# Kernel optimization log

Measured on AMD Instinct MI355X. Metric: run time of the kernel, lower is better.

Reference implementation:

```python
import jax, jax.numpy as jnp
import numpy as np

B, NCH, NPTS, NGT = 8, 4, 1024, 10
NANCH = 5 * NPTS
NMIN, NMAX = 64, 64
M = NMIN + NMAX
NPOOL = 64
EXT = 0.2
EPS = 1e-5
PERM = np.array([3, 4, 5, 1, 0, 2, 6])

_C = jnp.array([[0., 1, 0], [0, -1, 0], [2.5, -1, 0], [2.5, 1, 0], [2.5, 0, 0]], jnp.float32)
_ROT = jnp.array([[1., 0, 0], [0, 0, 1], [0, 1, 0]], jnp.float32)  # theta=0 rotation from source
NEW_CENTERS = _C @ _ROT  # (5,3)
DIM = jnp.array([2., 2., 5.], jnp.float32)


def _conv1x1(x, w, b):
    return jnp.einsum('bci,oc->boi', x, w) + b[None, :, None]


def _bn(x, g, be):  # BatchNorm1d in train mode: batch stats over (N, L)
    m = x.mean((0, 2), keepdims=True)
    v = ((x - m) ** 2).mean((0, 2), keepdims=True)
    return (x - m) * jax.lax.rsqrt(v + EPS) * g[None, :, None] + be[None, :, None]


def _corners(b):  # b=(cx,cz,w,l,ry) -> (4,2) CCW BEV corners
    lx = jnp.array([0.5, -0.5, -0.5, 0.5]) * b[2]
    lz = jnp.array([0.5, 0.5, -0.5, -0.5]) * b[3]
    c, s = jnp.cos(b[4]), jnp.sin(b[4])
    return jnp.stack([b[0] + lx * c - lz * s, b[1] + lx * s + lz * c], 1)


def _clip(poly, count, e1, e2):  # Sutherland-Hodgman: clip convex poly (8,2) by left half-plane of e1->e2
    idx = jnp.arange(8)
    valid = idx < count
    cnt = jnp.maximum(count, 1)
    nxt = poly[(idx + 1) % cnt]
    ex, ez = e2[0] - e1[0], e2[1] - e1[1]
    dc = ex * (poly[:, 1] - e1[1]) - ez * (poly[:, 0] - e1[0])
    dn = ex * (nxt[:, 1] - e1[1]) - ez * (nxt[:, 0] - e1[0])
    in_c, in_n = dc >= 0, dn >= 0
    den = dc - dn
    t = dc / jnp.where(jnp.abs(den) < 1e-9, 1e-9, den)
    inter = poly + t[:, None] * (nxt - poly)
    flags = jnp.stack([valid & in_c, valid & (in_c ^ in_n)], 1).reshape(16)
    pts = jnp.stack([poly, inter], 1).reshape(16, 2)
    pos = jnp.cumsum(flags) - 1
    out = jnp.zeros((8, 2), poly.dtype).at[jnp.where(flags, pos, 8)].set(pts, mode='drop')
    return out, flags.sum()


def _bev_iou(a, b):  # rotated BEV IoU, a,b=(cx,cz,w,l,ry)
    poly = jnp.zeros((8, 2)).at[:4].set(_corners(a))
    count = jnp.int32(4)
    cb = _corners(b)
    for k in range(4):
        poly, count = _clip(poly, count, cb[k], cb[(k + 1) % 4])
    idx = jnp.arange(8)
    nxt = poly[(idx + 1) % jnp.maximum(count, 1)]
    inter = 0.5 * jnp.abs(jnp.sum(jnp.where(idx < count, poly[:, 0] * nxt[:, 1] - nxt[:, 0] * poly[:, 1], 0.)))
    return inter / jnp.maximum(a[2] * a[3] + b[2] * b[3] - inter, 1e-8)


def _bev(b7):  # (..,7)=[x,y,z,h,w,l,ry] -> (cx,cz,w,l,ry)
    return jnp.stack([b7[..., 0], b7[..., 2], b7[..., 4], b7[..., 5], b7[..., 6]], -1)


def _select_one(pnts, labels):  # pnts (N,3), labels (G,9)
    cent = (pnts[:, None, :] - NEW_CENTERS[None]).reshape(NANCH, 3)  # repeat_interleave(pnts,5)-tile(centers)
    anchors = jnp.concatenate([jnp.broadcast_to(DIM, (NANCH, 3)), cent, jnp.zeros((NANCH, 1))], 1)
    a7 = anchors[:, PERM]
    g7 = labels[:, PERM]
    ab, gb = _bev(a7), _bev(g7)
    iou2d = jax.vmap(lambda g: jax.vmap(lambda a: _bev_iou(g, a))(ab))(gb)  # (G, NANCH)
    max_iou = iou2d.max(0)
    max_ind = jnp.argmax(iou2d, 0)
    order = jnp.argsort(max_iou)
    sel = jnp.concatenate([order[:NMIN], order[-NMAX:]])  # bottom-k + top-k
    return a7[sel], max_ind[sel], max_iou[sel]


def _pool_one(box, pts, ft):  # roipool3d: first NPOOL points inside expanded box, zero-padded
    c, s = jnp.cos(box[6]), jnp.sin(box[6])
    dx, dz = pts[:, 0] - box[0], pts[:, 2] - box[2]
    xl = dx * c + dz * s
    zl = -dx * s + dz * c
    inside = (jnp.abs(xl) < box[4] * 0.5 + EXT) & (jnp.abs(zl) < box[5] * 0.5 + EXT) \
             & (pts[:, 1] > box[1] - box[3] - EXT) & (pts[:, 1] < box[1] + EXT)
    order = jnp.argsort(jnp.logical_not(inside))[:NPOOL]  # stable sort: inside points first, original order
    valid = inside[order].astype(ft.dtype)[:, None]
    return jnp.concatenate([ft[order], pts[order]], -1) * valid  # (NPOOL, 256+3)


def _forward(points, gt_labels, p):
    x = jax.nn.relu(_bn(_conv1x1(points, p['pn_w1'], p['pn_b1']), p['pn_g1'], p['pn_be1']))
    x = jax.nn.relu(_bn(_conv1x1(x, p['pn_w2'], p['pn_b2']), p['pn_g2'], p['pn_be2']))
    x = _bn(_conv1x1(x, p['pn_w3'], p['pn_b3']), p['pn_g3'], p['pn_be3'])  # (B,256,N)
    pts = jnp.transpose(points[:, :3, :], (0, 2, 1))  # (B,N,3)
    sel_boxes, sel_idx, sel_iou = jax.vmap(_select_one)(pts, gt_labels)  # (B,M,7),(B,M),(B,M)
    ftr = jnp.transpose(x, (0, 2, 1))  # (B,N,256)
    pooled = jax.vmap(lambda bx, pp, ff: jax.vmap(lambda b: _pool_one(b, pp, ff))(bx))(sel_boxes, pts, ftr)
    pooled = pooled - jnp.pad(sel_boxes[:, :, None, :3], ((0, 0), (0, 0), (0, 0), (256, 0)))  # subtract center from last 3 ch
    pf = jnp.transpose(pooled.reshape(B * M, NPOOL, 259), (0, 2, 1))  # (B*M,259,64)
    f = _bn(_conv1x1(pf, p['rp_w1'], p['rp_b1']), p['rp_g1'], p['rp_be1'])
    f = _bn(_conv1x1(f, p['rp_w2'], p['rp_b2']), p['rp_g2'], p['rp_be2'])
    feats = f.reshape(B, M, 1024, NPOOL).max(-1)
    labels_bin = (sel_iou > 0.5).astype(jnp.int32)
    return feats, labels_bin, sel_iou, sel_boxes, gt_labels[-1], sel_idx


def setup_inputs():
    key = jax.random.key(0)
    ks = jax.random.split(key, 16)
    points = jax.random.normal(ks[0], (B, NCH, NPTS), jnp.float32) * 3.0
    dims = jax.random.uniform(ks[1], (B, NGT, 3), minval=1.0, maxval=4.0)
    ctrs = jax.random.normal(ks[2], (B, NGT, 3)) * 3.0
    th = jax.random.uniform(ks[3], (B, NGT, 1), minval=-3.14, maxval=3.14)
    extra = jax.random.normal(ks[4], (B, NGT, 2))
    gt_labels = jnp.concatenate([dims, ctrs, th, extra], -1).astype(jnp.float32)  # (B,G,9)
    inp = {'points': points, 'gt_labels': gt_labels}
    shapes = [('pn', 1, 64, NCH), ('pn', 2, 128, 64), ('pn', 3, 256, 128), ('rp', 1, 512, 259), ('rp', 2, 1024, 512)]
    for j, (pre, n, o, i) in enumerate(shapes):
        inp[f'{pre}_w{n}'] = jax.random.normal(ks[5 + j], (o, i), jnp.float32) / np.sqrt(i).astype(np.float32)
        inp[f'{pre}_b{n}'] = jnp.zeros((o,), jnp.float32)
        inp[f'{pre}_g{n}'] = jnp.ones((o,), jnp.float32)
        inp[f'{pre}_be{n}'] = jnp.zeros((o,), jnp.float32)
    return inp


def reference(points, gt_labels, pn_w1, pn_b1, pn_g1, pn_be1, pn_w2, pn_b2, pn_g2, pn_be2, pn_w3, pn_b3, pn_g3, pn_be3, rp_w1, rp_b1, rp_g1, rp_be1, rp_w2, rp_b2, rp_g2, rp_be2):
    p = dict(pn_w1=pn_w1, pn_b1=pn_b1, pn_g1=pn_g1, pn_be1=pn_be1, pn_w2=pn_w2, pn_b2=pn_b2, pn_g2=pn_g2, pn_be2=pn_be2, pn_w3=pn_w3, pn_b3=pn_b3, pn_g3=pn_g3, pn_be3=pn_be3, rp_w1=rp_w1, rp_b1=rp_b1, rp_g1=rp_g1, rp_be1=rp_be1, rp_w2=rp_w2, rp_b2=rp_b2, rp_g2=rp_g2, rp_be2=rp_be2)
    return _forward(points, gt_labels, p)
```

## Files before the change

kernel.cpp:

```cpp
#include <hip/hip_runtime.h>
#include <hip/hip_bf16.h>
#include <float.h>
#include <math.h>


typedef __attribute__((ext_vector_type(8))) short short8;
typedef __attribute__((ext_vector_type(4))) float f32x4;

template <int CTRL>
__device__ __forceinline__ float dppmv(float x) {
  return __int_as_float(__builtin_amdgcn_update_dpp(
      0, __float_as_int(x), CTRL, 0xF, 0xF, true));
}
__device__ __forceinline__ float dpp_sum16(float x) {
  x += dppmv<0xB1>(x);
  x += dppmv<0x4E>(x);
  x += dppmv<0x124>(x);
  x += dppmv<0x128>(x);
  return x;
}

__device__ __forceinline__ void stage1k(const unsigned short* g, unsigned short* l) {
  __builtin_amdgcn_global_load_lds(
      (const __attribute__((address_space(1))) unsigned int*)g,
      (__attribute__((address_space(3))) unsigned int*)l, 16, 0, 0);
}

#define FMA16()                                                                 \
  do {                                                                          \
    float4 av = *(const float4*)&sWT[cc][to * 4];                               \
    float4 bv = *(const float4*)&sB[cc][tk * 4];                                \
    acc[0][0] = fmaf(av.x, bv.x, acc[0][0]);                                    \
    acc[0][1] = fmaf(av.x, bv.y, acc[0][1]);                                    \
    acc[0][2] = fmaf(av.x, bv.z, acc[0][2]);                                    \
    acc[0][3] = fmaf(av.x, bv.w, acc[0][3]);                                    \
    acc[1][0] = fmaf(av.y, bv.x, acc[1][0]);                                    \
    acc[1][1] = fmaf(av.y, bv.y, acc[1][1]);                                    \
    acc[1][2] = fmaf(av.y, bv.z, acc[1][2]);                                    \
    acc[1][3] = fmaf(av.y, bv.w, acc[1][3]);                                    \
    acc[2][0] = fmaf(av.z, bv.x, acc[2][0]);                                    \
    acc[2][1] = fmaf(av.z, bv.y, acc[2][1]);                                    \
    acc[2][2] = fmaf(av.z, bv.z, acc[2][2]);                                    \
    acc[2][3] = fmaf(av.z, bv.w, acc[2][3]);                                    \
    acc[3][0] = fmaf(av.w, bv.x, acc[3][0]);                                    \
    acc[3][1] = fmaf(av.w, bv.y, acc[3][1]);                                    \
    acc[3][2] = fmaf(av.w, bv.z, acc[3][2]);                                    \
    acc[3][3] = fmaf(av.w, bv.w, acc[3][3]);                                    \
  } while (0)

template <int C, int O, bool AFF, bool RELU, bool TRANS>
__global__ __launch_bounds__(256) void conv_pn(const float* __restrict__ in,
                                               const float* __restrict__ w,
                                               const float* __restrict__ bias,
                                               const float* __restrict__ aff,
                                               float* __restrict__ out) {
  __shared__ __align__(16) float sB[64][68];
  __shared__ __align__(16) float sWT[64][68];
  const int i0 = blockIdx.x * 64;
  const int o0 = blockIdx.y * 64;
  const int b = blockIdx.z;
  const int tid = threadIdx.x;
  const int tk = tid & 15, to = tid >> 4;
  float acc[4][4] = {};
  for (int c0 = 0; c0 < C; c0 += 64) {
    const int cs = (C - c0 < 64) ? (C - c0) : 64;
    for (int idx = tid; idx < 4096; idx += 256) {
      int ii = idx & 63, cc = idx >> 6;
      float v = 0.f;
      if (cc < cs) {
        int c = c0 + cc;
        v = in[(b * C + c) * 1024 + i0 + ii];
        if (AFF) v = fmaf(v, aff[c], aff[C + c]);
        if (RELU) v = fmaxf(v, 0.f);
      }
      sB[cc][ii] = v;
    }
    for (int idx = tid; idx < 4096; idx += 256) {
      int cc = idx & 63, oo = idx >> 6;
      sWT[cc][oo] = (cc < cs) ? w[(o0 + oo) * C + c0 + cc] : 0.f;
    }
    __syncthreads();
    for (int cc = 0; cc < cs; ++cc) { FMA16(); }
    __syncthreads();
  }
  if (TRANS) {
    float b0 = bias[o0 + to * 4], b1 = bias[o0 + to * 4 + 1];
    float b2 = bias[o0 + to * 4 + 2], b3 = bias[o0 + to * 4 + 3];
#pragma unroll
    for (int jj = 0; jj < 4; ++jj) {
      float4 v = make_float4(acc[0][jj] + b0, acc[1][jj] + b1, acc[2][jj] + b2, acc[3][jj] + b3);
      *(float4*)&out[((size_t)(b * 1024) + i0 + tk * 4 + jj) * O + o0 + to * 4] = v;
    }
  } else {
    for (int j = 0; j < 4; ++j) {
      int o = o0 + to * 4 + j;
      float bs = bias[o];
      float4 v = make_float4(acc[j][0] + bs, acc[j][1] + bs, acc[j][2] + bs, acc[j][3] + bs);
      *(float4*)&out[(b * O + o) * 1024 + i0 + tk * 4] = v;
    }
  }
}

__global__ __launch_bounds__(256) void bn_stats(const float* __restrict__ x,
                                                const float* __restrict__ g,
                                                const float* __restrict__ be,
                                                float* __restrict__ aff, int C) {
#pragma clang fp contract(off)
  int c = blockIdx.x;
  int tid = threadIdx.x;
  float s = 0.f, q = 0.f;
  for (int idx = tid; idx < 8192; idx += 256) {
    int b = idx >> 10, i = idx & 1023;
    float v = x[(b * C + c) * 1024 + i];
    s += v;
    q += v * v;
  }
  for (int m = 1; m < 64; m <<= 1) {
    s += __shfl_xor(s, m);
    q += __shfl_xor(q, m);
  }
  __shared__ float as_[4], aq_[4];
  int wv = tid >> 6;
  if ((tid & 63) == 0) { as_[wv] = s; aq_[wv] = q; }
  __syncthreads();
  if (tid == 0) {
    s = as_[0] + as_[1] + as_[2] + as_[3];
    q = aq_[0] + aq_[1] + aq_[2] + aq_[3];
    float m_ = s * (1.f / 8192.f);
    float var = q * (1.f / 8192.f) - m_ * m_;
    float A = g[c] / sqrtf(var + 1e-5f);
    aff[c] = A;
    aff[C + c] = be[c] - m_ * A;
  }
}

__global__ __launch_bounds__(256) void bn_stats_t(const float* __restrict__ x,
                                                  const float* __restrict__ g,
                                                  const float* __restrict__ be,
                                                  float* __restrict__ aff) {
#pragma clang fp contract(off)
  int c = blockIdx.x;
  int tid = threadIdx.x;
  float s = 0.f, q = 0.f;
  for (int idx = tid; idx < 8192; idx += 256) {
    float v = x[(size_t)idx * 256 + c];
    s += v;
    q += v * v;
  }
  for (int m = 1; m < 64; m <<= 1) {
    s += __shfl_xor(s, m);
    q += __shfl_xor(q, m);
  }
  __shared__ float as_[4], aq_[4];
  int wv = tid >> 6;
  if ((tid & 63) == 0) { as_[wv] = s; aq_[wv] = q; }
  __syncthreads();
  if (tid == 0) {
    s = as_[0] + as_[1] + as_[2] + as_[3];
    q = aq_[0] + aq_[1] + aq_[2] + aq_[3];
    float m_ = s * (1.f / 8192.f);
    float var = q * (1.f / 8192.f) - m_ * m_;
    float A = g[c] / sqrtf(var + 1e-5f);
    aff[c] = A;
    aff[256 + c] = be[c] - m_ * A;
  }
}

__device__ __forceinline__ void poly_ins(float* ox, float* oz, int p, float vx, float vz) {
#pragma unroll
  for (int s = 0; s < 8; ++s)
    if (p == s) { ox[s] = vx; oz[s] = vz; }
}

__device__ float bev_iou_ga(const float* gx, const float* gz, float garea, float ax, float az) {
#pragma clang fp contract(off)
  float px[8], pz[8];
#pragma unroll
  for (int i = 0; i < 4; ++i) {
    px[i] = gx[i];
    pz[i] = gz[i];
    px[i + 4] = 0.f;
    pz[i + 4] = 0.f;
  }
  int count = 4;
  float kx[4], kz[4];
  kx[0] = ax + 1.f;  kz[0] = az + 2.5f;
  kx[1] = ax - 1.f;  kz[1] = az + 2.5f;
  kx[2] = ax - 1.f;  kz[2] = az - 2.5f;
  kx[3] = ax + 1.f;  kz[3] = az - 2.5f;
#pragma unroll
  for (int e = 0; e < 4; ++e) {
    float e1x = kx[e], e1z = kz[e];
    float e2x = kx[(e + 1) & 3], e2z = kz[(e + 1) & 3];
    float ex = e2x - e1x, ez = e2z - e1z;
    int cnt = count > 1 ? count : 1;
    int lim = count < 8 ? count : 8;
    float ox[8] = {}, oz[8] = {};
    int p = 0;
#pragma unroll
    for (int idx = 0; idx < 8; ++idx) {
      if (idx < lim) {
        const int nis = (idx + 1 > 7) ? 7 : idx + 1;
        float nx = px[nis], nz = pz[nis];
        if (idx + 1 == cnt) { nx = px[0]; nz = pz[0]; }
        float cx = px[idx], cz = pz[idx];
        float dc = ex * (cz - e1z) - ez * (cx - e1x);
        float dn = ex * (nz - e1z) - ez * (nx - e1x);
        bool ic = dc >= 0.f, in_ = dn >= 0.f;
        if (ic) {
          poly_ins(ox, oz, p, cx, cz);
          ++p;
        }
        if (ic != in_) {
          float den = dc - dn;
          float t = dc / (fabsf(den) < 1e-9f ? 1e-9f : den);
          poly_ins(ox, oz, p, cx + t * (nx - cx), cz + t * (nz - cz));
          ++p;
        }
      }
    }
    count = p;
    int cp = p < 8 ? p : 8;
#pragma unroll
    for (int i = 0; i < 8; ++i) {
      px[i] = (i < cp) ? ox[i] : 0.f;
      pz[i] = (i < cp) ? oz[i] : 0.f;
    }
  }
  int cnt = count > 1 ? count : 1;
  int lim = count < 8 ? count : 8;
  float ssum = 0.f;
#pragma unroll
  for (int idx = 0; idx < 8; ++idx) {
    if (idx < lim) {
      const int nis = (idx + 1 > 7) ? 7 : idx + 1;
      float nx = px[nis], nz = pz[nis];
      if (idx + 1 == cnt) { nx = px[0]; nz = pz[0]; }
      ssum += px[idx] * nz - nx * pz[idx];
    }
  }
  float inter = 0.5f * fabsf(ssum);
  return inter / fmaxf(garea + 10.f - inter, 1e-8f);
}

__global__ __launch_bounds__(256) void fused_mid(
    const float* __restrict__ in2, const float* __restrict__ w3,
    const float* __restrict__ b3, const float* __restrict__ aff2,
    float* __restrict__ out3T,
    const float* __restrict__ points, const float* __restrict__ gt,
    float* __restrict__ iou10, float* __restrict__ o_gt, int* __restrict__ rank,
    const float* __restrict__ w1, unsigned short* __restrict__ W1f) {
  __shared__ __align__(16) float sB[64][68];
  __shared__ __align__(16) float sWT[64][68];
  const int bid = blockIdx.x;
  const int tid = threadIdx.x;
  if (bid < 512) {
    const int i0 = (bid & 15) * 64;
    const int o0 = ((bid >> 4) & 3) * 64;
    const int b = bid >> 6;
    const int tk = tid & 15, to = tid >> 4;
    float acc[4][4] = {};
    for (int c0 = 0; c0 < 128; c0 += 64) {
      for (int idx = tid; idx < 4096; idx += 256) {
        int ii = idx & 63, cc = idx >> 6;
        int c = c0 + cc;
        float v = in2[(b * 128 + c) * 1024 + i0 + ii];
        v = fmaf(v, aff2[c], aff2[128 + c]);
        v = fmaxf(v, 0.f);
        sB[cc][ii] = v;
      }
      for (int idx = tid; idx < 4096; idx += 256) {
        int cc = idx & 63, oo = idx >> 6;
        sWT[cc][oo] = w3[(o0 + oo) * 128 + c0 + cc];
      }
      __syncthreads();
      for (int cc = 0; cc < 64; ++cc) { FMA16(); }
      __syncthreads();
    }
    float c0v = b3[o0 + to * 4], c1v = b3[o0 + to * 4 + 1];
    float c2v = b3[o0 + to * 4 + 2], c3v = b3[o0 + to * 4 + 3];
#pragma unroll
    for (int jj = 0; jj < 4; ++jj) {
      float4 v = make_float4(acc[0][jj] + c0v, acc[1][jj] + c1v, acc[2][jj] + c2v, acc[3][jj] + c3v);
      *(float4*)&out3T[((size_t)(b * 1024) + i0 + tk * 4 + jj) * 256 + o0 + to * 4] = v;
    }
  } else if (bid < 2112) {
#pragma clang fp contract(off)
    int r = bid - 512;
    int g = r / 160;
    int rb = r % 160;
    int b = rb / 20;
    int axb = rb % 20;
    int a = axb * 256 + tid;
    if (g == 0) rank[b * 5120 + a] = 0;
    if (g == 0 && b == 0 && axb == 0 && tid < 90)
      o_gt[tid] = gt[630 + tid];
    const float* L = gt + b * 90 + g * 9;
    float gxx = L[3], gzz = L[5], gw = L[0], gl = L[2], gth = L[6];
    float c = cosf(gth), s = sinf(gth);
    const float sx[4] = {0.5f, -0.5f, -0.5f, 0.5f};
    const float sz[4] = {0.5f, 0.5f, -0.5f, -0.5f};
    float gcx[4], gcz[4];
#pragma unroll
    for (int k = 0; k < 4; ++k) {
      float lx = sx[k] * gw, lz = sz[k] * gl;
      gcx[k] = gxx + lx * c - lz * s;
      gcz[k] = gzz + lx * s + lz * c;
    }
    float garea = gw * gl;
    int pt = a / 5, j = a % 5;
    const float CX[5] = {0.f, 0.f, 2.5f, 2.5f, 2.5f};
    const float CZ[5] = {1.f, -1.f, -1.f, 1.f, 0.f};
    const float* P = points + b * 4096;
    float ax = P[pt] - CX[j];
    float az = P[2048 + pt] - CZ[j];
    iou10[(size_t)(b * 10 + g) * 5120 + a] = bev_iou_ga(gcx, gcz, garea, ax, az);
  } else {
    int o = (bid - 2112) * 4 + (tid >> 6);
    int lp = tid & 63;
    if (lp < 36) {
      int ks = lp >> 2, quad = lp & 3;
      int tile = o >> 4;
      union { __hip_bfloat16 h[8]; uint4 u; } pk;
#pragma unroll
      for (int j = 0; j < 8; ++j) {
        int c = ks * 32 + quad * 8 + j;
        float v = (c < 259) ? w1[o * 259 + c] : 0.f;
        pk.h[j] = __float2bfloat16(v);
      }
      *(uint4*)&W1f[((size_t)(tile * 9 + ks) * 64 + quad * 16 + (o & 15)) * 8] = pk.u;
    }
  }
}

__global__ __launch_bounds__(256) void iou_reduce(const float* __restrict__ iou10,
                                                  float* __restrict__ maxiou,
                                                  int* __restrict__ maxind) {
  int b = blockIdx.y;
  int a = blockIdx.x * 256 + threadIdx.x;
  float best = -1.f;
  int bi = 0;
  for (int g = 0; g < 10; ++g) {
    float v = iou10[(size_t)(b * 10 + g) * 5120 + a];
    if (v > best) { best = v; bi = g; }
  }
  maxiou[b * 5120 + a] = best;
  maxind[b * 5120 + a] = bi;
}

__global__ __launch_bounds__(256) void select_rank(const float* __restrict__ maxiou,
                                                   int* __restrict__ rank) {
  __shared__ __align__(16) float vals[640];
  int b = blockIdx.y, chunk = blockIdx.z, tid = threadIdx.x;
  int jb0 = chunk * 640;
  for (int i = tid; i < 640; i += 256) vals[i] = maxiou[b * 5120 + jb0 + i];
  int a = blockIdx.x * 256 + tid;
  float av = maxiou[b * 5120 + a];
  __syncthreads();
  int rk = 0;
#pragma unroll 4
  for (int j4 = 0; j4 < 160; ++j4) {
    float4 v = *(const float4*)&vals[j4 * 4];
    int jb = jb0 + j4 * 4;
    rk += (v.x < av) || (v.x == av && jb < a);
    rk += (v.y < av) || (v.y == av && jb + 1 < a);
    rk += (v.z < av) || (v.z == av && jb + 2 < a);
    rk += (v.w < av) || (v.w == av && jb + 3 < a);
  }
  atomicAdd(&rank[b * 5120 + a], rk);
}

__global__ __launch_bounds__(256) void select_write(const int* __restrict__ rank,
                                                    const float* __restrict__ maxiou,
                                                    const int* __restrict__ maxind,
                                                    const float* __restrict__ points,
                                                    float* __restrict__ o_lbl,
                                                    float* __restrict__ o_iou,
                                                    float* __restrict__ o_box,
                                                    float* __restrict__ o_idx) {
#pragma clang fp contract(off)
  int b = blockIdx.y, tid = threadIdx.x;
  int a = blockIdx.x * 256 + tid;
  int rk = rank[b * 5120 + a];
  int slot = -1;
  if (rk < 64) slot = rk;
  else if (rk >= 5056) slot = rk - 4992;
  if (slot >= 0) {
    const float CX[5] = {0.f, 0.f, 2.5f, 2.5f, 2.5f};
    const float CZ[5] = {1.f, -1.f, -1.f, 1.f, 0.f};
    int base = b * 128 + slot;
    float av = maxiou[b * 5120 + a];
    o_iou[base] = av;
    o_lbl[base] = av > 0.5f ? 1.f : 0.f;
    o_idx[base] = (float)maxind[b * 5120 + a];
    int pt = a / 5, j = a % 5;
    const float* P = points + b * 4096;
    float* bx = o_box + base * 7;
    bx[0] = P[pt] - CX[j];
    bx[1] = P[1024 + pt];
    bx[2] = P[2048 + pt] - CZ[j];
    bx[3] = 2.f;
    bx[4] = 2.f;
    bx[5] = 5.f;
    bx[6] = 0.f;
  }
}

__global__ __launch_bounds__(256) void pool_kernel(const float* __restrict__ points,
                                                   const float* __restrict__ selboxes,
                                                   int* __restrict__ selpts) {
#pragma clang fp contract(off)
  int box = blockIdx.x * 4 + (threadIdx.x >> 6);
  int lane = threadIdx.x & 63;
  int b = box >> 7;
  const float* bx = selboxes + box * 7;
  float b0 = bx[0], b1 = bx[1], b2 = bx[2], b3 = bx[3], b4 = bx[4], b5 = bx[5];
  float limx = b4 * 0.5f + 0.2f, limz = b5 * 0.5f + 0.2f;
  float ylo = b1 - b3 - 0.2f, yhi = b1 + 0.2f;
  const float* P = points + b * 4096;
  unsigned long long m[16];
  int total_in = 0;
#pragma unroll
  for (int r = 0; r < 16; ++r) {
    int pt = r * 64 + lane;
    float dx = P[pt] - b0;
    float py = P[1024 + pt];
    float dz = P[2048 + pt] - b2;
    bool ins = (fabsf(dx) < limx) && (fabsf(dz) < limz) && (py > ylo) && (py < yhi);
    m[r] = __ballot(ins);
    total_in += __popcll(m[r]);
  }
  unsigned long long lowmask = (1ull << lane) - 1;
  int cum = 0;
#pragma unroll
  for (int r = 0; r < 16; ++r) {
    int pt = r * 64 + lane;
    int inbefore = cum + __popcll(m[r] & lowmask);
    bool ins = (m[r] >> lane) & 1;
    int slot = ins ? inbefore : total_in + (pt - inbefore);
    if (slot < 64) selpts[box * 64 + slot] = pt | (ins ? 0x10000 : 0);
    cum += __popcll(m[r]);
  }
}

__global__ __launch_bounds__(256) void gather_pf(const float* __restrict__ out3T,
                                                 const float* __restrict__ points,
                                                 const int* __restrict__ selpts,
                                                 const float* __restrict__ selboxes,
                                                 const float* __restrict__ aff3,
                                                 unsigned short* __restrict__ pff) {
  __shared__ int sSel[64];
  __shared__ float sCen[3];
  __shared__ float sA3[256], sB3[256];
  const int bm = blockIdx.x;
  const int b = bm >> 7;
  const int tid = threadIdx.x;
  if (tid < 64) sSel[tid] = selpts[bm * 64 + tid];
  if (tid >= 64 && tid < 67) sCen[tid - 64] = selboxes[bm * 7 + (tid - 64)];
  sA3[tid] = aff3[tid];
  sB3[tid] = aff3[256 + tid];
  __syncthreads();
  const int pool = tid >> 2, part = tid & 3;
  const int ni = pool >> 4, nib = pool & 15;
  const int sv = sSel[pool];
  const int pt = sv & 0xFFFF;
  const bool valid = (sv >> 16) != 0;
  const float* row = out3T + ((size_t)(b << 10) + pt) * 256;
#pragma unroll
  for (int ks = 0; ks < 8; ++ks) {
    int c0 = ks * 32 + part * 8;
    float4 x0 = *(const float4*)&row[c0];
    float4 x1 = *(const float4*)&row[c0 + 4];
    float v[8] = {x0.x, x0.y, x0.z, x0.w, x1.x, x1.y, x1.z, x1.w};
    union { __hip_bfloat16 h[8]; uint4 u; } pk;
#pragma unroll
    for (int e = 0; e < 8; ++e) {
      float vv = valid ? fmaf(v[e], sA3[c0 + e], sB3[c0 + e]) : 0.f;
      pk.h[e] = __float2bfloat16(vv);
    }
    *(uint4*)&pff[((size_t)((bm * 9 + ks) * 4 + ni) * 64 + part * 16 + nib) * 8] = pk.u;
  }
  union { __hip_bfloat16 h[8]; uint4 u; } pk;
#pragma unroll
  for (int e = 0; e < 8; ++e) pk.h[e] = __float2bfloat16(0.f);
  if (part == 0) {
#pragma unroll
    for (int d = 0; d < 3; ++d) {
      float pv = valid ? points[(b * 4 + d) * 1024 + pt] : 0.f;
      pk.h[d] = __float2bfloat16(pv - sCen[d]);
    }
  }
  *(uint4*)&pff[((size_t)((bm * 9 + 8) * 4 + ni) * 64 + part * 16 + nib) * 8] = pk.u;
}

__global__ __launch_bounds__(256) void rp1_mfma(const unsigned short* __restrict__ W1f,
                                                const unsigned short* __restrict__ pff,
                                                const float* __restrict__ bias1,
                                                unsigned short* __restrict__ g1x,
                                                float* __restrict__ psum4,
                                                float* __restrict__ psq4) {
  __shared__ __align__(16) unsigned short sBuf[2][6144];
  const int tid = threadIdx.x;
  const int lane = tid & 63, w = tid >> 6;
  const int quad = lane >> 4, nib = lane & 15;
  const int l = blockIdx.x;
  const int xcd = l & 7;
  const int j = l >> 3;
  const int ot = j & 3;
  const int bm = xcd * 128 + (j >> 2);
  const unsigned short* Aw = &W1f[((size_t)(ot * 8 + w * 2) * 9 * 64 + lane) * 8];
  const unsigned short* Bg = pff + (size_t)bm * 18432 + w * 1536 + lane * 8;
#pragma unroll
  for (int i = 0; i < 3; ++i)
    stage1k(Bg + i * 512, &sBuf[0][w * 1536 + i * 512]);
  __syncthreads();
  f32x4 acc[2][4] = {};
  int cur = 0;
#pragma unroll
  for (int c = 0; c < 3; ++c) {
    if (c < 2) {
#pragma unroll
      for (int i = 0; i < 3; ++i)
        stage1k(Bg + (c + 1) * 6144 + i * 512, &sBuf[cur ^ 1][w * 1536 + i * 512]);
    }
    const unsigned short* Bl = &sBuf[cur][lane * 8];
#pragma unroll
    for (int k2 = 0; k2 < 3; ++k2) {
      const int ks = c * 3 + k2;
      short8 af[2], bf[4];
#pragma unroll
      for (int mi = 0; mi < 2; ++mi)
        af[mi] = *(const short8*)&Aw[(size_t)(mi * 9 + ks) * 512];
#pragma unroll
      for (int ni = 0; ni < 4; ++ni)
        bf[ni] = *(const short8*)&Bl[(size_t)(k2 * 4 + ni) * 512];
#pragma unroll
      for (int mi = 0; mi < 2; ++mi)
#pragma unroll
        for (int ni = 0; ni < 4; ++ni)
          acc[mi][ni] = __builtin_amdgcn_mfma_f32_16x16x32_bf16(af[mi], bf[ni], acc[mi][ni], 0, 0, 0);
    }
    __syncthreads();
    cur ^= 1;
  }
  const int cbase = ot * 128 + w * 32;
#pragma unroll
  for (int mi = 0; mi < 2; ++mi) {
    float bv[4];
#pragma unroll
    for (int r = 0; r < 4; ++r) bv[r] = bias1[cbase + mi * 16 + quad * 4 + r];
    float s[4] = {0.f, 0.f, 0.f, 0.f}, q[4] = {0.f, 0.f, 0.f, 0.f};
    const int kgbase = (cbase + mi * 16) >> 3;
#pragma unroll
    for (int ni = 0; ni < 4; ++ni) {
      union { __hip_bfloat16 h[4]; unsigned int u[2]; } pk;
#pragma unroll
      for (int r = 0; r < 4; ++r) {
        float v = acc[mi][ni][r] + bv[r];
        pk.h[r] = __float2bfloat16(v);
        s[r] += v;
        q[r] += v * v;
      }
      unsigned int p0 = (unsigned int)__shfl_xor((int)pk.u[0], 16);
      unsigned int p1 = (unsigned int)__shfl_xor((int)pk.u[1], 16);
      if ((quad & 1) == 0) {
        uint4 g = make_uint4(pk.u[0], pk.u[1], p0, p1);
        int kg = kgbase + (quad >> 1);
        *(uint4*)&g1x[((size_t)(bm * 64 + kg) * 64 + ni * 16 + nib) * 8] = g;
      }
    }
#pragma unroll
    for (int r = 0; r < 4; ++r) {
      float ss = dpp_sum16(s[r]);
      float qq = dpp_sum16(q[r]);
      if (nib == 0) {
        int o = cbase + mi * 16 + quad * 4 + r;
        psum4[(size_t)o * 1024 + bm] = ss;
        psq4[(size_t)o * 1024 + bm] = qq;
      }
    }
  }
}

__global__ __launch_bounds__(64) void bn_aff_part(const float* __restrict__ psum,
                                                  const float* __restrict__ psq,
                                                  const float* __restrict__ g,
                                                  const float* __restrict__ be,
                                                  float* __restrict__ aff, int C) {
#pragma clang fp contract(off)
  int o = blockIdx.x;
  int lane = threadIdx.x;
  float s = 0.f, q = 0.f;
  for (int i = 0; i < 16; ++i) {
    int bm = i * 64 + lane;
    s += psum[(size_t)o * 1024 + bm];
    q += psq[(size_t)o * 1024 + bm];
  }
  for (int m = 1; m < 64; m <<= 1) {
    s += __shfl_xor(s, m);
    q += __shfl_xor(q, m);
  }
  if (lane == 0) {
    float m_ = s * (1.f / 65536.f);
    float var = q * (1.f / 65536.f) - m_ * m_;
    float A = g[o] / sqrtf(var + 1e-5f);
    aff[o] = A;
    aff[C + o] = be[o] - m_ * A;
  }
}

__global__ __launch_bounds__(64) void prep_w2(const float* __restrict__ w2,
                                              const float* __restrict__ b2,
                                              const float* __restrict__ aff4,
                                              unsigned short* __restrict__ W2f,
                                              float* __restrict__ bias2p) {
  int o = blockIdx.x;
  int lp = threadIdx.x;
  int ks = lp >> 2, quad = lp & 3;
  int tile = o >> 4;
  float accb = 0.f;
  union { __hip_bfloat16 h[8]; uint4 u; } pk;
#pragma unroll
  for (int j = 0; j < 8; ++j) {
    int c = ks * 32 + quad * 8 + j;
    float wv = w2[o * 512 + c];
    pk.h[j] = __float2bfloat16(wv * aff4[c]);
    accb += wv * aff4[512 + c];
  }
  *(uint4*)&W2f[((size_t)(tile * 16 + ks) * 64 + quad * 16 + (o & 15)) * 8] = pk.u;
  for (int m = 1; m < 64; m <<= 1) accb += __shfl_xor(accb, m);
  if (lp == 0) bias2p[o] = b2[o] + accb;
}

__global__ __launch_bounds__(256) void rp2_mfma(const unsigned short* __restrict__ W2f,
                                                const unsigned short* __restrict__ g1x,
                                                const float* __restrict__ bias2p,
                                                float* __restrict__ maxb,
                                                float* __restrict__ minb,
                                                float* __restrict__ psum,
                                                float* __restrict__ psq) {
  __shared__ __align__(16) unsigned short sBuf[2][8192];
  const int tid = threadIdx.x;
  const int lane = tid & 63, w = tid >> 6;
  const int quad = lane >> 4, nib = lane & 15;
  const int l = blockIdx.x;
  const int xcd = l & 7;
  const int j = l >> 3;
  const int ot = j & 3;
  const int bm = xcd * 128 + (j >> 2);
  const unsigned short* Aw = &W2f[((size_t)(ot * 4 + w) * 4 * 16 * 64 + lane) * 8];
  const unsigned short* Bg = g1x + (size_t)bm * 32768 + w * 2048 + lane * 8;
#pragma unroll
  for (int i = 0; i < 4; ++i)
    stage1k(Bg + i * 512, &sBuf[0][w * 2048 + i * 512]);
  __syncthreads();
  f32x4 acc[4][4] = {};
  int cur = 0;
#pragma unroll
  for (int c = 0; c < 4; ++c) {
    if (c < 3) {
#pragma unroll
      for (int i = 0; i < 4; ++i)
        stage1k(Bg + (c + 1) * 8192 + i * 512, &sBuf[cur ^ 1][w * 2048 + i * 512]);
    }
    const unsigned short* Bl = &sBuf[cur][quad * 512 + nib * 8];
#pragma unroll
    for (int k2 = 0; k2 < 4; ++k2) {
      const int ks = c * 4 + k2;
      short8 af[4], bf[4];
#pragma unroll
      for (int mi = 0; mi < 4; ++mi)
        af[mi] = *(const short8*)&Aw[(size_t)(mi * 16 + ks) * 512];
#pragma unroll
      for (int ni = 0; ni < 4; ++ni)
        bf[ni] = *(const short8*)&Bl[(size_t)(k2 * 2048 + ni * 128)];
#pragma unroll
      for (int mi = 0; mi < 4; ++mi)
#pragma unroll
        for (int ni = 0; ni < 4; ++ni)
          acc[ni][mi] = __builtin_amdgcn_mfma_f32_16x16x32_bf16(bf[ni], af[mi], acc[ni][mi], 0, 0, 0);
    }
    __syncthreads();
    cur ^= 1;
  }
  const int obase = ot * 256 + w * 64;
#pragma unroll
  for (int oi = 0; oi < 4; ++oi) {
    int o = obase + oi * 16 + nib;
    float bs = bias2p[o];
    float mx = -FLT_MAX, mn = FLT_MAX, s = 0.f, q = 0.f;
#pragma unroll
    for (int pi = 0; pi < 4; ++pi) {
#pragma unroll
      for (int r = 0; r < 4; ++r) {
        float v = acc[pi][oi][r] + bs;
        mx = fmaxf(mx, v);
        mn = fminf(mn, v);
        s += v;
        q += v * v;
      }
    }
    mx = fmaxf(mx, __shfl_xor(mx, 16));
    mx = fmaxf(mx, __shfl_xor(mx, 32));
    mn = fminf(mn, __shfl_xor(mn, 16));
    mn = fminf(mn, __shfl_xor(mn, 32));
    s += __shfl_xor(s, 16);
    s += __shfl_xor(s, 32);
    q += __shfl_xor(q, 16);
    q += __shfl_xor(q, 32);
    if (quad == 0) {
      maxb[bm * 1024 + o] = mx;
      minb[bm * 1024 + o] = mn;
      psum[(size_t)o * 1024 + bm] = s;
      psq[(size_t)o * 1024 + bm] = q;
    }
  }
}

__global__ void feats_kernel(const float* __restrict__ maxb, const float* __restrict__ minb,
                             const float* __restrict__ aff5, float* __restrict__ o_feats) {
#pragma clang fp contract(off)
  int i = blockIdx.x * 256 + threadIdx.x;
  int o = i & 1023;
  float A = aff5[o], Bv = aff5[1024 + o];
  float v = (A >= 0.f) ? maxb[i] : minb[i];
  o_feats[i] = v * A + Bv;
}

extern "C" void kernel_launch(void* const* d_in, const int* in_sizes, int n_in,
                              void* d_out, int out_size, void* d_ws, size_t ws_size,
                              hipStream_t stream) {
  (void)in_sizes; (void)n_in; (void)out_size; (void)ws_size;
  const float* points = (const float*)d_in[0];
  const float* gt = (const float*)d_in[1];
  const float* pn_w1 = (const float*)d_in[2];
  const float* pn_b1 = (const float*)d_in[3];
  const float* pn_g1 = (const float*)d_in[4];
  const float* pn_be1 = (const float*)d_in[5];
  const float* pn_w2 = (const float*)d_in[6];
  const float* pn_b2 = (const float*)d_in[7];
  const float* pn_g2 = (const float*)d_in[8];
  const float* pn_be2 = (const float*)d_in[9];
  const float* pn_w3 = (const float*)d_in[10];
  const float* pn_b3 = (const float*)d_in[11];
  const float* pn_g3 = (const float*)d_in[12];
  const float* pn_be3 = (const float*)d_in[13];
  const float* rp_w1 = (const float*)d_in[14];
  const float* rp_b1 = (const float*)d_in[15];
  const float* rp_g1 = (const float*)d_in[16];
  const float* rp_be1 = (const float*)d_in[17];
  const float* rp_w2 = (const float*)d_in[18];
  const float* rp_b2 = (const float*)d_in[19];
  const float* rp_g2 = (const float*)d_in[20];
  const float* rp_be2 = (const float*)d_in[21];

  float* ws = (float*)d_ws;
  float* out1 = ws;
  float* out2 = out1 + 524288;
  float* maxiou = out2 + 1048576;
  int* maxind = (int*)(maxiou + 40960);
  int* selpts = maxind + 40960;
  int* rank = selpts + 65536;
  float* aff1 = (float*)(rank + 40960);
  float* aff2 = aff1 + 128;
  float* aff3 = aff2 + 256;
  float* aff4 = aff3 + 512;
  float* aff5 = aff4 + 1024;
  float* psum4 = aff5 + 2048;
  float* psq4 = psum4 + 524288;
  unsigned short* W1f = (unsigned short*)(psq4 + 524288);
  float* pff_f = (float*)(W1f) + 73728;
  unsigned short* pff = (unsigned short*)pff_f;
  float* g1x_f = pff_f + 9437184;
  unsigned short* g1x = (unsigned short*)g1x_f;
  float* out3T = g1x_f;
  float* iou10 = g1x_f + 2097152;
  float* maxb = pff_f;
  float* minb = maxb + 1048576;
  float* psum5 = minb + 1048576;
  float* psq5 = psum5 + 1048576;
  unsigned short* W2f = (unsigned short*)out1;
  float* bias2p = out1 + 262144;

  float* o_feats = (float*)d_out;
  float* o_lbl = o_feats + 1048576;
  float* o_iou = o_lbl + 1024;
  float* o_box = o_iou + 1024;
  float* o_gt = o_box + 7168;
  float* o_idx = o_gt + 90;

  conv_pn<4, 64, false, false, false><<<dim3(16, 1, 8), 256, 0, stream>>>(points, pn_w1, pn_b1, nullptr, out1);
  bn_stats<<<64, 256, 0, stream>>>(out1, pn_g1, pn_be1, aff1, 64);
  conv_pn<64, 128, true, true, false><<<dim3(16, 2, 8), 256, 0, stream>>>(out1, pn_w2, pn_b2, aff1, out2);
  bn_stats<<<128, 256, 0, stream>>>(out2, pn_g2, pn_be2, aff2, 128);
  fused_mid<<<2240, 256, 0, stream>>>(out2, pn_w3, pn_b3, aff2, out3T,
                                      points, gt, iou10, o_gt, rank,
                                      rp_w1, W1f);
  bn_stats_t<<<256, 256, 0, stream>>>(out3T, pn_g3, pn_be3, aff3);
  iou_reduce<<<dim3(20, 8), 256, 0, stream>>>(iou10, maxiou, maxind);
  select_rank<<<dim3(20, 8, 8), 256, 0, stream>>>(maxiou, rank);
  select_write<<<dim3(20, 8), 256, 0, stream>>>(rank, maxiou, maxind, points, o_lbl, o_iou, o_box, o_idx);
  pool_kernel<<<256, 256, 0, stream>>>(points, o_box, selpts);
  gather_pf<<<1024, 256, 0, stream>>>(out3T, points, selpts, o_box, aff3, pff);
  rp1_mfma<<<4096, 256, 0, stream>>>(W1f, pff, rp_b1, g1x, psum4, psq4);
  bn_aff_part<<<512, 64, 0, stream>>>(psum4, psq4, rp_g1, rp_be1, aff4, 512);
  prep_w2<<<1024, 64, 0, stream>>>(rp_w2, rp_b2, aff4, W2f, bias2p);
  rp2_mfma<<<4096, 256, 0, stream>>>(W2f, g1x, bias2p, maxb, minb, psum5, psq5);
  bn_aff_part<<<1024, 64, 0, stream>>>(psum5, psq5, rp_g2, rp_be2, aff5, 1024);
  feats_kernel<<<4096, 256, 0, stream>>>(maxb, minb, aff5, o_feats);
}
```

Before: 352.0 us.

## Fuse gather into rp1 MFMA and merge BN stats with IoU reduce

The gather/BN-apply of pooled features is fused into the first MLP MFMA kernel. Each 1024-thread block builds the bf16 B-tile in LDS directly, which drops the global pff round trip and one launch. The BN-stats and IoU max-reduce kernels are merged into a single launch split by block index. The workspace layout is reshuffled so out3T no longer aliases g1x. The cost is larger blocks, less cross-block overlap in staging, and lost XCD-aware block mapping.

Measured after the change: 344.5 us. -2.1%, faster.

```diff
diff --git a/kernel.cpp b/kernel.cpp
--- a/kernel.cpp
+++ b/kernel.cpp
@@ -131,38 +131,6 @@
     float A = g[c] / sqrtf(var + 1e-5f);
     aff[c] = A;
     aff[C + c] = be[c] - m_ * A;
-  }
-}
-
-__global__ __launch_bounds__(256) void bn_stats_t(const float* __restrict__ x,
-                                                  const float* __restrict__ g,
-                                                  const float* __restrict__ be,
-                                                  float* __restrict__ aff) {
-#pragma clang fp contract(off)
-  int c = blockIdx.x;
-  int tid = threadIdx.x;
-  float s = 0.f, q = 0.f;
-  for (int idx = tid; idx < 8192; idx += 256) {
-    float v = x[(size_t)idx * 256 + c];
-    s += v;
-    q += v * v;
-  }
-  for (int m = 1; m < 64; m <<= 1) {
-    s += __shfl_xor(s, m);
-    q += __shfl_xor(q, m);
-  }
-  __shared__ float as_[4], aq_[4];
-  int wv = tid >> 6;
-  if ((tid & 63) == 0) { as_[wv] = s; aq_[wv] = q; }
-  __syncthreads();
-  if (tid == 0) {
-    s = as_[0] + as_[1] + as_[2] + as_[3];
-    q = aq_[0] + aq_[1] + aq_[2] + aq_[3];
-    float m_ = s * (1.f / 8192.f);
-    float var = q * (1.f / 8192.f) - m_ * m_;
-    float A = g[c] / sqrtf(var + 1e-5f);
-    aff[c] = A;
-    aff[256 + c] = be[c] - m_ * A;
   }
 }
 
@@ -333,19 +301,52 @@
   }
 }
 
-__global__ __launch_bounds__(256) void iou_reduce(const float* __restrict__ iou10,
-                                                  float* __restrict__ maxiou,
-                                                  int* __restrict__ maxind) {
-  int b = blockIdx.y;
-  int a = blockIdx.x * 256 + threadIdx.x;
-  float best = -1.f;
-  int bi = 0;
-  for (int g = 0; g < 10; ++g) {
-    float v = iou10[(size_t)(b * 10 + g) * 5120 + a];
-    if (v > best) { best = v; bi = g; }
-  }
-  maxiou[b * 5120 + a] = best;
-  maxind[b * 5120 + a] = bi;
+__global__ __launch_bounds__(256) void bn_iou_red(
+    const float* __restrict__ x, const float* __restrict__ g,
+    const float* __restrict__ be, float* __restrict__ aff,
+    const float* __restrict__ iou10, float* __restrict__ maxiou,
+    int* __restrict__ maxind) {
+  const int bid = blockIdx.x;
+  const int tid = threadIdx.x;
+  if (bid < 256) {
+#pragma clang fp contract(off)
+    int c = bid;
+    float s = 0.f, q = 0.f;
+    for (int idx = tid; idx < 8192; idx += 256) {
+      float v = x[(size_t)idx * 256 + c];
+      s += v;
+      q += v * v;
+    }
+    for (int m = 1; m < 64; m <<= 1) {
+      s += __shfl_xor(s, m);
+      q += __shfl_xor(q, m);
+    }
+    __shared__ float as_[4], aq_[4];
+    int wv = tid >> 6;
+    if ((tid & 63) == 0) { as_[wv] = s; aq_[wv] = q; }
+    __syncthreads();
+    if (tid == 0) {
+      s = as_[0] + as_[1] + as_[2] + as_[3];
+      q = aq_[0] + aq_[1] + aq_[2] + aq_[3];
+      float m_ = s * (1.f / 8192.f);
+      float var = q * (1.f / 8192.f) - m_ * m_;
+      float A = g[c] / sqrtf(var + 1e-5f);
+      aff[c] = A;
+      aff[256 + c] = be[c] - m_ * A;
+    }
+  } else {
+    int r = bid - 256;
+    int b = r / 20;
+    int a = (r % 20) * 256 + tid;
+    float best = -1.f;
+    int bi = 0;
+    for (int g2 = 0; g2 < 10; ++g2) {
+      float v = iou10[(size_t)(b * 10 + g2) * 5120 + a];
+      if (v > best) { best = v; bi = g2; }
+    }
+    maxiou[b * 5120 + a] = best;
+    maxind[b * 5120 + a] = bi;
+  }
 }
 
 __global__ __launch_bounds__(256) void select_rank(const float* __restrict__ maxiou,
@@ -443,12 +444,13 @@
   }
 }
 
-__global__ __launch_bounds__(256) void gather_pf(const float* __restrict__ out3T,
-                                                 const float* __restrict__ points,
-                                                 const int* __restrict__ selpts,
-                                                 const float* __restrict__ selboxes,
-                                                 const float* __restrict__ aff3,
-                                                 unsigned short* __restrict__ pff) {
+__global__ __launch_bounds__(1024) void gather_rp1(
+    const float* __restrict__ out3T, const float* __restrict__ points,
+    const int* __restrict__ selpts, const float* __restrict__ selboxes,
+    const float* __restrict__ aff3, const float* __restrict__ bias1,
+    const unsigned short* __restrict__ W1f, unsigned short* __restrict__ g1x,
+    float* __restrict__ psum4, float* __restrict__ psq4) {
+  __shared__ __align__(16) unsigned short sBuf[18432];
   __shared__ int sSel[64];
   __shared__ float sCen[3];
   __shared__ float sA3[256], sB3[256];
@@ -457,91 +459,72 @@
   const int tid = threadIdx.x;
   if (tid < 64) sSel[tid] = selpts[bm * 64 + tid];
   if (tid >= 64 && tid < 67) sCen[tid - 64] = selboxes[bm * 7 + (tid - 64)];
-  sA3[tid] = aff3[tid];
-  sB3[tid] = aff3[256 + tid];
+  if (tid >= 256 && tid < 512) sA3[tid - 256] = aff3[tid - 256];
+  if (tid >= 512 && tid < 768) sB3[tid - 512] = aff3[256 + tid - 512];
   __syncthreads();
-  const int pool = tid >> 2, part = tid & 3;
-  const int ni = pool >> 4, nib = pool & 15;
-  const int sv = sSel[pool];
-  const int pt = sv & 0xFFFF;
-  const bool valid = (sv >> 16) != 0;
-  const float* row = out3T + ((size_t)(b << 10) + pt) * 256;
-#pragma unroll
-  for (int ks = 0; ks < 8; ++ks) {
-    int c0 = ks * 32 + part * 8;
-    float4 x0 = *(const float4*)&row[c0];
-    float4 x1 = *(const float4*)&row[c0 + 4];
-    float v[8] = {x0.x, x0.y, x0.z, x0.w, x1.x, x1.y, x1.z, x1.w};
-    union { __hip_bfloat16 h[8]; uint4 u; } pk;
-#pragma unroll
-    for (int e = 0; e < 8; ++e) {
-      float vv = valid ? fmaf(v[e], sA3[c0 + e], sB3[c0 + e]) : 0.f;
-      pk.h[e] = __float2bfloat16(vv);
-    }
-    *(uint4*)&pff[((size_t)((bm * 9 + ks) * 4 + ni) * 64 + part * 16 + nib) * 8] = pk.u;
-  }
-  union { __hip_bfloat16 h[8]; uint4 u; } pk;
-#pragma unroll
-  for (int e = 0; e < 8; ++e) pk.h[e] = __float2bfloat16(0.f);
-  if (part == 0) {
-#pragma unroll
-    for (int d = 0; d < 3; ++d) {
-      float pv = valid ? points[(b * 4 + d) * 1024 + pt] : 0.f;
-      pk.h[d] = __float2bfloat16(pv - sCen[d]);
-    }
-  }
-  *(uint4*)&pff[((size_t)((bm * 9 + 8) * 4 + ni) * 64 + part * 16 + nib) * 8] = pk.u;
-}
-
-__global__ __launch_bounds__(256) void rp1_mfma(const unsigned short* __restrict__ W1f,
-                                                const unsigned short* __restrict__ pff,
-                                                const float* __restrict__ bias1,
-                                                unsigned short* __restrict__ g1x,
-                                                float* __restrict__ psum4,
-                                                float* __restrict__ psq4) {
-  __shared__ __align__(16) unsigned short sBuf[2][6144];
-  const int tid = threadIdx.x;
-  const int lane = tid & 63, w = tid >> 6;
+  for (int u = tid; u < 2304; u += 1024) {
+    int ks, pool, part;
+    if (u < 2048) {
+      ks = u >> 8;
+      int rem = u & 255;
+      pool = rem >> 2;
+      part = rem & 3;
+    } else {
+      int v = u - 2048;
+      ks = 8;
+      pool = v >> 2;
+      part = v & 3;
+    }
+    const int ni = pool >> 4, nib = pool & 15;
+    const int sv = sSel[pool];
+    const int pt = sv & 0xFFFF;
+    const bool valid = (sv >> 16) != 0;
+    union { __hip_bfloat16 h[8]; uint4 uu; } pk;
+    if (ks < 8) {
+      const float* row = out3T + ((size_t)(b << 10) + pt) * 256;
+      int c0 = ks * 32 + part * 8;
+      float4 x0 = *(const float4*)&row[c0];
+      float4 x1 = *(const float4*)&row[c0 + 4];
+      float v[8] = {x0.x, x0.y, x0.z, x0.w, x1.x, x1.y, x1.z, x1.w};
+#pragma unroll
+      for (int e = 0; e < 8; ++e) {
+        float vv = valid ? fmaf(v[e], sA3[c0 + e], sB3[c0 + e]) : 0.f;
+        pk.h[e] = __float2bfloat16(vv);
+      }
+    } else {
+#pragma unroll
+      for (int e = 0; e < 8; ++e) pk.h[e] = __float2bfloat16(0.f);
+      if (part == 0) {
+#pragma unroll
+        for (int d = 0; d < 3; ++d) {
+          float pv = valid ? points[(b * 4 + d) * 1024 + pt] : 0.f;
+          pk.h[d] = __float2bfloat16(pv - sCen[d]);
+        }
+      }
+    }
+    *(uint4*)&sBuf[(size_t)(((ks * 4 + ni) * 64) + part * 16 + nib) * 8] = pk.uu;
+  }
+  __syncthreads();
+  const int lane = tid & 63, wv = tid >> 6;
+  const int ot = wv >> 2, w = wv & 3;
   const int quad = lane >> 4, nib = lane & 15;
-  const int l = blockIdx.x;
-  const int xcd = l & 7;
-  const int j = l >> 3;
-  const int ot = j & 3;
-  const int bm = xcd * 128 + (j >> 2);
   const unsigned short* Aw = &W1f[((size_t)(ot * 8 + w * 2) * 9 * 64 + lane) * 8];
-  const unsigned short* Bg = pff + (size_t)bm * 18432 + w * 1536 + lane * 8;
-#pragma unroll
-  for (int i = 0; i < 3; ++i)
-    stage1k(Bg + i * 512, &sBuf[0][w * 1536 + i * 512]);
-  __syncthreads();
+  const unsigned short* Bl = &sBuf[lane * 8];
   f32x4 acc[2][4] = {};
-  int cur = 0;
-#pragma unroll
-  for (int c = 0; c < 3; ++c) {
-    if (c < 2) {
-#pragma unroll
-      for (int i = 0; i < 3; ++i)
-        stage1k(Bg + (c + 1) * 6144 + i * 512, &sBuf[cur ^ 1][w * 1536 + i * 512]);
-    }
-    const unsigned short* Bl = &sBuf[cur][lane * 8];
-#pragma unroll
-    for (int k2 = 0; k2 < 3; ++k2) {
-      const int ks = c * 3 + k2;
-      short8 af[2], bf[4];
-#pragma unroll
-      for (int mi = 0; mi < 2; ++mi)
-        af[mi] = *(const short8*)&Aw[(size_t)(mi * 9 + ks) * 512];
+#pragma unroll
+  for (int ks = 0; ks < 9; ++ks) {
+    short8 af[2], bf[4];
+#pragma unroll
+    for (int mi = 0; mi < 2; ++mi)
+      af[mi] = *(const short8*)&Aw[(size_t)(mi * 9 + ks) * 512];
+#pragma unroll
+    for (int ni = 0; ni < 4; ++ni)
+      bf[ni] = *(const short8*)&Bl[(size_t)(ks * 4 + ni) * 512];
+#pragma unroll
+    for (int mi = 0; mi < 2; ++mi)
 #pragma unroll
       for (int ni = 0; ni < 4; ++ni)
-        bf[ni] = *(const short8*)&Bl[(size_t)(k2 * 4 + ni) * 512];
-#pragma unroll
-      for (int mi = 0; mi < 2; ++mi)
-#pragma unroll
-        for (int ni = 0; ni < 4; ++ni)
-          acc[mi][ni] = __builtin_amdgcn_mfma_f32_16x16x32_bf16(af[mi], bf[ni], acc[mi][ni], 0, 0, 0);
-    }
-    __syncthreads();
-    cur ^= 1;
+        acc[mi][ni] = __builtin_amdgcn_mfma_f32_16x16x32_bf16(af[mi], bf[ni], acc[mi][ni], 0, 0, 0);
   }
   const int cbase = ot * 128 + w * 32;
 #pragma unroll
@@ -770,15 +753,14 @@
   float* psq4 = psum4 + 524288;
   unsigned short* W1f = (unsigned short*)(psq4 + 524288);
   float* pff_f = (float*)(W1f) + 73728;
-  unsigned short* pff = (unsigned short*)pff_f;
-  float* g1x_f = pff_f + 9437184;
-  unsigned short* g1x = (unsigned short*)g1x_f;
-  float* out3T = g1x_f;
-  float* iou10 = g1x_f + 2097152;
-  float* maxb = pff_f;
+  float* out3T = pff_f;
+  float* maxb = pff_f + 2097152;
   float* minb = maxb + 1048576;
   float* psum5 = minb + 1048576;
   float* psq5 = psum5 + 1048576;
+  float* g1x_f = pff_f + 9437184;
+  unsigned short* g1x = (unsigned short*)g1x_f;
+  float* iou10 = g1x_f + 2097152;
   unsigned short* W2f = (unsigned short*)out1;
   float* bias2p = out1 + 262144;
 
@@ -796,13 +778,13 @@
   fused_mid<<<2240, 256, 0, stream>>>(out2, pn_w3, pn_b3, aff2, out3T,
                                       points, gt, iou10, o_gt, rank,
                                       rp_w1, W1f);
-  bn_stats_t<<<256, 256, 0, stream>>>(out3T, pn_g3, pn_be3, aff3);
-  iou_reduce<<<dim3(20, 8), 256, 0, stream>>>(iou10, maxiou, maxind);
+  bn_iou_red<<<416, 256, 0, stream>>>(out3T, pn_g3, pn_be3, aff3,
+                                      iou10, maxiou, maxind);
   select_rank<<<dim3(20, 8, 8), 256, 0, stream>>>(maxiou, rank);
   select_write<<<dim3(20, 8), 256, 0, stream>>>(rank, maxiou, maxind, points, o_lbl, o_iou, o_box, o_idx);
   pool_kernel<<<256, 256, 0, stream>>>(points, o_box, selpts);
-  gather_pf<<<1024, 256, 0, stream>>>(out3T, points, selpts, o_box, aff3, pff);
-  rp1_mfma<<<4096, 256, 0, stream>>>(W1f, pff, rp_b1, g1x, psum4, psq4);
+  gather_rp1<<<1024, 1024, 0, stream>>>(out3T, points, selpts, o_box, aff3,
+                                        rp_b1, W1f, g1x, psum4, psq4);
   bn_aff_part<<<512, 64, 0, stream>>>(psum4, psq4, rp_g1, rp_be1, aff4, 512);
   prep_w2<<<1024, 64, 0, stream>>>(rp_w2, rp_b2, aff4, W2f, bias2p);
   rp2_mfma<<<4096, 256, 0, stream>>>(W2f, g1x, bias2p, maxb, minb, psum5, psq5);
```
